# Kernel tuning notes

Measured on AMD Instinct MI355X. Metric: run time of the kernel, lower is better.

Reference implementation:

```python
import jax, jax.numpy as jnp
import numpy as np
import math

B, L, D, P = 2, 2048, 256, 32
PI = math.pi


def _layernorm(x, g, b, eps=1e-5):
    m = x.mean(-1, keepdims=True)
    v = x.var(-1, keepdims=True)
    return (x - m) / jnp.sqrt(v + eps) * g + b


def setup_inputs() -> dict:
    key = jax.random.key(0)
    ks = jax.random.split(key, 16)
    sd = 1.0 / math.sqrt(D)
    f32 = jnp.float32
    inp = {
        "x": jax.random.normal(ks[0], (B, L, D), f32),
        # key_encoder: Linear(D, P)
        "key_W": jax.random.normal(ks[1], (D, P), f32) * sd,
        "key_b": jnp.zeros((P,), f32),
        # value_encoder: Linear(D, D)
        "val_W": jax.random.normal(ks[2], (D, D), f32) * sd,
        "val_b": jnp.zeros((D,), f32),
        # refiner: LayerNorm(D), Linear(D, 2D), GELU, Linear(2D, D)
        "ln1_g": jnp.ones((D,), f32),
        "ln1_b": jnp.zeros((D,), f32),
        "W1": jax.random.normal(ks[3], (D, 2 * D), f32) * sd,
        "b1": jnp.zeros((2 * D,), f32),
        "W2": jax.random.normal(ks[4], (2 * D, D), f32) * (1.0 / math.sqrt(2 * D)),
        "b2": jnp.zeros((D,), f32),
        # to_out: LayerNorm(D), Linear(D, D)
        "ln2_g": jnp.ones((D,), f32),
        "ln2_b": jnp.zeros((D,), f32),
        "Wo": jax.random.normal(ks[5], (D, D), f32) * sd,
        "bo": jnp.zeros((D,), f32),
    }
    return inp


def reference(x, key_W, key_b, val_W, val_b, ln1_g, ln1_b, W1, b1, W2, b2,
              ln2_g, ln2_b, Wo, bo):
    # key phases in (-pi, pi); phasor exp(i*theta) handled as (cos, sin)
    phases = jnp.tanh(x @ key_W + key_b) * PI          # (B, L, P)
    values = x @ val_W + val_b                          # (B, L, D)

    cos_p = jnp.cos(phases)
    sin_p = jnp.sin(phases)
    # torch.roll(shifts=1, dims=1) then zero the first position -> shift right, row 0 = 0
    zrow = jnp.zeros_like(cos_p[:, :1])
    cos_s = jnp.concatenate([zrow, cos_p[:, :-1]], axis=1)
    sin_s = jnp.concatenate([zrow, sin_p[:, :-1]], axis=1)

    # odd positions hold values
    vmask = (jnp.arange(L) % 2 == 1).astype(x.dtype)    # (L,)
    mv = values * vmask[None, :, None]                  # (B, L, D)

    # bind: outer product phasor (P) x value (D); real/imag parts
    bound_re = cos_s[..., None] * mv[:, :, None, :]     # (B, L, P, D)
    bound_im = sin_s[..., None] * mv[:, :, None, :]
    mem_re = jnp.cumsum(bound_re, axis=1)
    mem_im = jnp.cumsum(bound_im, axis=1)

    # retrieve: Re[ memory * exp(-i*theta) ] summed over phases
    retrieved = (jnp.einsum('blpd,blp->bld', mem_re, cos_p)
                 + jnp.einsum('blpd,blp->bld', mem_im, sin_p))

    valid = jnp.maximum(jnp.cumsum(vmask), 1.0)         # (L,)
    retrieved = retrieved / (jnp.sqrt(valid)[None, :, None] * math.sqrt(P))

    h = _layernorm(retrieved, ln1_g, ln1_b)
    h = jax.nn.gelu(h @ W1 + b1, approximate=False)
    refined = h @ W2 + b2
    out = x + (_layernorm(refined, ln2_g, ln2_b) @ Wo + bo)
    return out
```

## Files before the change

kernel.cpp:

```cpp
#include <hip/hip_runtime.h>
#include <math.h>

#define BB 2
#define LL 2048
#define DD 256
#define PP 32
#define NC 64
#define PI_F 3.14159265358979323846f

typedef __attribute__((ext_vector_type(8))) short bf16x8;
typedef __attribute__((ext_vector_type(4))) float f32x4;
typedef unsigned short ushort_t;
typedef unsigned int uint_t;

__device__ inline ushort_t f2bf(float x) {
    uint_t u = __float_as_uint(x);
    uint_t r = (u + 0x7fffu + ((u >> 16) & 1u)) >> 16;
    return (ushort_t)r;
}

__global__ __launch_bounds__(256) void prep_key_kernel(
    const float* __restrict__ W1, const float* __restrict__ W2,
    const float* __restrict__ Wo, const float* __restrict__ valW,
    const float* __restrict__ x, const float* __restrict__ key_W,
    const float* __restrict__ key_b,
    ushort_t* __restrict__ W1t, ushort_t* __restrict__ W2t,
    ushort_t* __restrict__ Wot, ushort_t* __restrict__ valWt,
    float2* __restrict__ ph)
{
    const int bid = blockIdx.x;
    const int t = threadIdx.x;
    if (bid < 96) {
        __shared__ float T[64][65];
        const float* W; ushort_t* Wt; int K, N, tile;
        if (bid < 32)      { W = W1;   Wt = W1t;   K = 256; N = 512; tile = bid; }
        else if (bid < 64) { W = W2;   Wt = W2t;   K = 512; N = 256; tile = bid - 32; }
        else if (bid < 80) { W = Wo;   Wt = Wot;   K = 256; N = 256; tile = bid - 64; }
        else               { W = valW; Wt = valWt; K = 256; N = 256; tile = bid - 80; }
        const int ntiles = N / 64;
        const int k0 = (tile / ntiles) * 64, n0 = (tile % ntiles) * 64;
        {
            const int rr = t >> 2, cb = (t & 3) * 16;
            #pragma unroll
            for (int i = 0; i < 16; i += 4) {
                const float4 v = *(const float4*)&W[(k0 + rr) * N + n0 + cb + i];
                T[rr][cb + i + 0] = v.x; T[rr][cb + i + 1] = v.y;
                T[rr][cb + i + 2] = v.z; T[rr][cb + i + 3] = v.w;
            }
        }
        __syncthreads();
        {
            const int n = t >> 2, kb = (t & 3) * 16;
            #pragma unroll
            for (int i = 0; i < 16; ++i)
                Wt[(n0 + n) * K + k0 + kb + i] = f2bf(T[kb + i][n]);
        }
    } else {
        __shared__ ushort_t xt[16][264];
        __shared__ ushort_t kwT[32][264];
        __shared__ float rbuf[4][2][16][17];
        const int row0 = (bid - 96) * 16;
        {
            const int l = t >> 4, cb = (t & 15) * 16;
            const float* src = &x[(long)(row0 + l) * DD + cb];
            ushort_t tmp[16];
            #pragma unroll
            for (int i = 0; i < 4; ++i) {
                const float4 v = *(const float4*)&src[i * 4];
                tmp[i*4+0] = f2bf(v.x); tmp[i*4+1] = f2bf(v.y);
                tmp[i*4+2] = f2bf(v.z); tmp[i*4+3] = f2bf(v.w);
            }
            *(uint4*)&xt[l][cb]     = *(uint4*)&tmp[0];
            *(uint4*)&xt[l][cb + 8] = *(uint4*)&tmp[8];
        }
        {
            #pragma unroll
            for (int i = 0; i < 8; ++i) {
                const int idx4 = i * 256 + t;
                const int k = idx4 >> 3, pc = (idx4 & 7) * 4;
                const float4 v = *(const float4*)&key_W[k * 32 + pc];
                kwT[pc + 0][k] = f2bf(v.x);
                kwT[pc + 1][k] = f2bf(v.y);
                kwT[pc + 2][k] = f2bf(v.z);
                kwT[pc + 3][k] = f2bf(v.w);
            }
        }
        __syncthreads();
        const int wv = t >> 6, lane = t & 63;
        const int qd = lane >> 4, mc = lane & 15;
        f32x4 acc0 = {0.f,0.f,0.f,0.f}, acc1 = {0.f,0.f,0.f,0.f};
        #pragma unroll
        for (int ks = 0; ks < 2; ++ks) {
            const int ko = wv * 64 + ks * 32 + qd * 8;
            const bf16x8 a  = *(const bf16x8*)&xt[mc][ko];
            const bf16x8 b0 = *(const bf16x8*)&kwT[mc][ko];
            const bf16x8 b1 = *(const bf16x8*)&kwT[16 + mc][ko];
            acc0 = __builtin_amdgcn_mfma_f32_16x16x32_bf16(a, b0, acc0, 0, 0, 0);
            acc1 = __builtin_amdgcn_mfma_f32_16x16x32_bf16(a, b1, acc1, 0, 0, 0);
        }
        #pragma unroll
        for (int r = 0; r < 4; ++r) {
            rbuf[wv][0][qd * 4 + r][mc] = acc0[r];
            rbuf[wv][1][qd * 4 + r][mc] = acc1[r];
        }
        __syncthreads();
        #pragma unroll
        for (int rep = 0; rep < 2; ++rep) {
            const int idx = rep * 256 + t;
            const int p = idx & 31, l = idx >> 5;
            const int nf = p >> 4, mcol = p & 15;
            float a = key_b[p] + rbuf[0][nf][l][mcol] + rbuf[1][nf][l][mcol]
                    + rbuf[2][nf][l][mcol] + rbuf[3][nf][l][mcol];
            a = tanhf(a) * PI_F;
            float sn, cs;
            sincosf(a, &sn, &cs);
            ph[(long)(row0 + l) * PP + p] = make_float2(cs, sn);
        }
    }
}

__global__ __launch_bounds__(256) void valbind_kernel(
    const float* __restrict__ x, const float2* __restrict__ ph,
    const ushort_t* __restrict__ valWt, const float* __restrict__ val_b,
    ushort_t* __restrict__ VoddT, float* __restrict__ Mt)
{
    __shared__ ushort_t xsb[16][264];
    __shared__ ushort_t VdT[64][40];
    __shared__ ushort_t phsT[64][40];
    __shared__ float    Ms[64][68];

    const int tid = threadIdx.x;
    const int bid = blockIdx.x;
    const int b  = bid >> 8;
    const int c  = (bid >> 2) & 63;
    const int dq = bid & 3;
    const int base = b * LL;
    const int r0 = 32 * c;

    {
        const int j = tid >> 4, cb = (tid & 15) * 16;
        const float* src = &x[(long)(base + r0 + 2 * j + 1) * DD + cb];
        ushort_t tmp[16];
        #pragma unroll
        for (int i = 0; i < 4; ++i) {
            const float4 v = *(const float4*)&src[i * 4];
            tmp[i*4+0] = f2bf(v.x); tmp[i*4+1] = f2bf(v.y);
            tmp[i*4+2] = f2bf(v.z); tmp[i*4+3] = f2bf(v.w);
        }
        *(uint4*)&xsb[j][cb]     = *(uint4*)&tmp[0];
        *(uint4*)&xsb[j][cb + 8] = *(uint4*)&tmp[8];
    }
    {
        const int j = tid >> 4, qb = (tid & 15) * 4;
        const float4 v = *(const float4*)((const float*)ph +
                              (long)(base + r0 + 2 * j) * 64 + qb);
        phsT[qb + 0][j] = f2bf(v.x);
        phsT[qb + 1][j] = f2bf(v.y);
        phsT[qb + 2][j] = f2bf(v.z);
        phsT[qb + 3][j] = f2bf(v.w);
    }
    for (int e = tid; e < 64 * 16; e += 256) {
        phsT[e >> 4][16 + (e & 15)] = 0;
        VdT[e >> 4][16 + (e & 15)] = 0;
    }
    __syncthreads();

    const int wv = tid >> 6, lane = tid & 63;
    const int qd = lane >> 4, mc = lane & 15;

    f32x4 va = {0.f,0.f,0.f,0.f};
    const int dloc = wv * 16 + mc;
    const int ng = dq * 64 + dloc;
    const ushort_t* B0 = &valWt[(long)ng * 256];
    #pragma unroll
    for (int ks = 0; ks < 8; ++ks) {
        const bf16x8 a  = *(const bf16x8*)&xsb[mc][ks * 32 + qd * 8];
        const bf16x8 b0 = *(const bf16x8*)&B0[ks * 32 + qd * 8];
        va = __builtin_amdgcn_mfma_f32_16x16x32_bf16(a, b0, va, 0, 0, 0);
    }
    {
        const float bb = val_b[ng];
        #pragma unroll
        for (int r = 0; r < 4; ++r)
            VdT[dloc][qd * 4 + r] = f2bf(va[r] + bb);
    }
    __syncthreads();

    const bf16x8 a2 = *(const bf16x8*)&phsT[wv * 16 + mc][qd * 8];
    f32x4 macc[4];
    #pragma unroll
    for (int nf = 0; nf < 4; ++nf) {
        f32x4 z = {0.f,0.f,0.f,0.f};
        const bf16x8 b2 = *(const bf16x8*)&VdT[nf * 16 + mc][qd * 8];
        macc[nf] = __builtin_amdgcn_mfma_f32_16x16x32_bf16(a2, b2, z, 0, 0, 0);
    }
    #pragma unroll
    for (int nf = 0; nf < 4; ++nf) {
        #pragma unroll
        for (int r = 0; r < 4; ++r)
            Ms[nf * 16 + mc][wv * 16 + qd * 4 + r] = macc[nf][r];
    }
    __syncthreads();

    {
        float* dst = &Mt[((long)(b * NC + c) * 256 + dq * 64) * 64];
        #pragma unroll
        for (int p = 0; p < 4; ++p) {
            const int idx4 = p * 256 + tid;
            const int dl = idx4 >> 4, q4 = (idx4 & 15) * 4;
            *(float4*)&dst[dl * 64 + q4] = *(const float4*)&Ms[dl][q4];
        }
    }
    if (tid < 64) {
        ushort_t* vd = &VoddT[((long)(b * NC + c) * 256 + dq * 64 + tid) * 16];
        *(uint4*)&vd[0] = *(const uint4*)&VdT[tid][0];
        *(uint4*)&vd[8] = *(const uint4*)&VdT[tid][8];
    }
}

__global__ __launch_bounds__(256) void prefix_kernel(
    const float* __restrict__ M, ushort_t* __restrict__ Mpre_b)
{
    __shared__ float segsum[4][64];
    const int tid = threadIdx.x;
    const int b  = blockIdx.x >> 8;
    const int cg = blockIdx.x & 255;
    const int col = cg * 64 + (tid & 63);
    const int seg = tid >> 6;
    const long base = (long)b * NC * 16384 + col;

    float v[16], s = 0.f;
    #pragma unroll
    for (int i = 0; i < 16; ++i) {
        v[i] = M[base + (long)(seg * 16 + i) * 16384];
        s += v[i];
    }
    segsum[seg][tid & 63] = s;
    __syncthreads();
    float run = 0.f;
    #pragma unroll
    for (int sg = 0; sg < 3; ++sg)
        if (sg < seg) run += segsum[sg][tid & 63];
    #pragma unroll
    for (int i = 0; i < 16; ++i) {
        const long a = base + (long)(seg * 16 + i) * 16384;
        Mpre_b[a] = f2bf(run);
        run += v[i];
    }
}

__global__ __launch_bounds__(512) void retrieve_mlp_kernel(
    const float* __restrict__ ph, const ushort_t* __restrict__ Mpre_b,
    const ushort_t* __restrict__ VoddT,
    const float* __restrict__ ln1_g, const float* __restrict__ ln1_b,
    const ushort_t* __restrict__ W1t, const float* __restrict__ b1,
    const ushort_t* __restrict__ W2t, const float* __restrict__ b2,
    const float* __restrict__ ln2_g, const float* __restrict__ ln2_b,
    const ushort_t* __restrict__ Wot, const float* __restrict__ bo,
    const float* __restrict__ x, float* __restrict__ out)
{
    __shared__ ushort_t Bs_m[256][72];
    __shared__ ushort_t Bs_v[256][32];
    __shared__ ushort_t As_ph[16][72];
    __shared__ ushort_t Bs_sh[16][72];
    __shared__ ushort_t As_p[16][32];
    __shared__ float    refct[16][264];
    __shared__ ushort_t rhat_s[16][264];
    __shared__ ushort_t h_s[16][520];
    __shared__ ushort_t shT[16][264];

    const int tid = threadIdx.x;
    const int b = blockIdx.x >> 7;
    const int c = (blockIdx.x >> 1) & 63;
    const int h = blockIdx.x & 1;
    const int l0g = 32 * c + 16 * h;
    const long rowbase = (long)b * LL + l0g;

    {
        const ushort_t* src = &Mpre_b[(long)(b * NC + c) * 16384];
        #pragma unroll
        for (int p = 0; p < 4; ++p) {
            const int idx8 = p * 512 + tid;
            const int d = idx8 >> 3, q8 = (idx8 & 7) * 8;
            *(uint4*)&Bs_m[d][q8] = *(const uint4*)&src[idx8 * 8];
        }
    }
    if (tid < 256) {
        const int r = tid >> 4, q4 = (tid & 15) * 4;
        const float4 vv = *(const float4*)((const float*)ph + (rowbase + r) * 64 + q4);
        ushort_t t0[4] = {f2bf(vv.x), f2bf(vv.y), f2bf(vv.z), f2bf(vv.w)};
        *(uint2*)&As_ph[r][q4] = *(uint2*)t0;
        const float4 w = *(const float4*)((const float*)ph +
                             ((long)b * LL + 32 * c + 2 * r) * 64 + q4);
        ushort_t t1[4] = {f2bf(w.x), f2bf(w.y), f2bf(w.z), f2bf(w.w)};
        *(uint2*)&Bs_sh[r][q4] = *(uint2*)t1;
    }
    {
        const ushort_t* src = &VoddT[(long)(b * NC + c) * 4096];
        const int j0 = (tid & 1) * 8;
        *(uint4*)&Bs_v[tid >> 1][j0] = *(const uint4*)&src[tid * 8];
        *(uint4*)&Bs_v[tid >> 1][16 + j0] = make_uint4(0, 0, 0, 0);
        if (tid < 256) As_p[tid >> 4][16 + (tid & 15)] = 0;
    }
    __syncthreads();

    const int wv = tid >> 6, lane = tid & 63;
    const int qd = lane >> 4, mc = lane & 15;

    {
        f32x4 sacc = {0.f, 0.f, 0.f, 0.f};
        #pragma unroll
        for (int ks = 0; ks < 2; ++ks) {
            const bf16x8 a  = *(const bf16x8*)&As_ph[mc][ks * 32 + qd * 8];
            const bf16x8 bb = *(const bf16x8*)&Bs_sh[mc][ks * 32 + qd * 8];
            sacc = __builtin_amdgcn_mfma_f32_16x16x32_bf16(a, bb, sacc, 0, 0, 0);
        }
        if (wv == 0) {
            #pragma unroll
            for (int r = 0; r < 4; ++r) {
                const int l = qd * 4 + r;
                As_p[l][mc] = (2 * mc + 1 <= 16 * h + l) ? f2bf(sacc[r])
                                                         : (ushort_t)0;
            }
        }
    }

    f32x4 acc[2];
    #pragma unroll
    for (int i = 0; i < 2; ++i) acc[i] = (f32x4){0.f, 0.f, 0.f, 0.f};
    #pragma unroll
    for (int i = 0; i < 2; ++i) {
        const int d0 = wv * 32 + i * 16;
        #pragma unroll
        for (int ks = 0; ks < 2; ++ks) {
            const bf16x8 a  = *(const bf16x8*)&As_ph[mc][ks * 32 + qd * 8];
            const bf16x8 bb = *(const bf16x8*)&Bs_m[d0 + mc][ks * 32 + qd * 8];
            acc[i] = __builtin_amdgcn_mfma_f32_16x16x32_bf16(a, bb, acc[i], 0, 0, 0);
        }
    }
    __syncthreads();

    {
        const bf16x8 a2 = *(const bf16x8*)&As_p[mc][qd * 8];
        #pragma unroll
        for (int i = 0; i < 2; ++i) {
            const int d0 = wv * 32 + i * 16;
            const bf16x8 b2 = *(const bf16x8*)&Bs_v[d0 + mc][qd * 8];
            acc[i] = __builtin_amdgcn_mfma_f32_16x16x32_bf16(a2, b2, acc[i], 0, 0, 0);
        }
    }

    #pragma unroll
    for (int r = 0; r < 4; ++r) {
        const int l = qd * 4 + r;
        int va = (l0g + l + 1) >> 1; if (va < 1) va = 1;
        const float sc = 0.17677669529663687f * rsqrtf((float)va);
        #pragma unroll
        for (int i = 0; i < 2; ++i)
            refct[l][wv * 32 + i * 16 + mc] = acc[i][r] * sc;
    }
    __syncthreads();

    {
        const int row = tid >> 5, cg = (tid & 31) * 8;
        float s = 0.f, sq = 0.f;
        #pragma unroll
        for (int i = 0; i < 8; ++i) {
            const float v = refct[row][cg + i];
            s += v; sq += v * v;
        }
        s += __shfl_xor(s, 1, 32);  sq += __shfl_xor(sq, 1, 32);
        s += __shfl_xor(s, 2, 32);  sq += __shfl_xor(sq, 2, 32);
        s += __shfl_xor(s, 4, 32);  sq += __shfl_xor(sq, 4, 32);
        s += __shfl_xor(s, 8, 32);  sq += __shfl_xor(sq, 8, 32);
        s += __shfl_xor(s, 16, 32); sq += __shfl_xor(sq, 16, 32);
        const float m = s * (1.f / 256.f);
        const float inv = rsqrtf(sq * (1.f / 256.f) - m * m + 1e-5f);
        ushort_t o16[8];
        #pragma unroll
        for (int i = 0; i < 8; ++i) {
            const int cc = cg + i;
            o16[i] = f2bf((refct[row][cc] - m) * inv * ln1_g[cc] + ln1_b[cc]);
        }
        *(uint4*)&rhat_s[row][cg] = *(uint4*)&o16[0];
    }

    #pragma unroll
    for (int nh = 0; nh < 2; ++nh) {
        f32x4 acc1[2];
        #pragma unroll
        for (int nf = 0; nf < 2; ++nf) acc1[nf] = (f32x4){0.f,0.f,0.f,0.f};
        for (int k0 = 0; k0 < 256; k0 += 64) {
            __syncthreads();
            {
                const int sk = (tid & 7) * 8;
                #pragma unroll
                for (int rr = 0; rr < 4; ++rr) {
                    const int n = rr * 64 + (tid >> 3);
                    *(uint4*)&Bs_m[n][sk] =
                        *(const uint4*)&W1t[(long)(nh * 256 + n) * 256 + k0 + sk];
                }
            }
            __syncthreads();
            #pragma unroll
            for (int ks = 0; ks < 2; ++ks) {
                const bf16x8 a = *(const bf16x8*)&rhat_s[mc][k0 + ks * 32 + qd * 8];
                #pragma unroll
                for (int nf = 0; nf < 2; ++nf) {
                    const bf16x8 bb = *(const bf16x8*)&Bs_m[wv * 32 + nf * 16 + mc][ks * 32 + qd * 8];
                    acc1[nf] = __builtin_amdgcn_mfma_f32_16x16x32_bf16(a, bb, acc1[nf], 0, 0, 0);
                }
            }
        }
        #pragma unroll
        for (int nf = 0; nf < 2; ++nf) {
            const int n = nh * 256 + wv * 32 + nf * 16 + mc;
            const float bb = b1[n];
            #pragma unroll
            for (int r = 0; r < 4; ++r) {
                float v = acc1[nf][r] + bb;
                v = 0.5f * v * (1.f + erff(v * 0.70710678118654752f));
                h_s[qd * 4 + r][n] = f2bf(v);
            }
        }
    }

    f32x4 acc2[2];
    #pragma unroll
    for (int nf = 0; nf < 2; ++nf) acc2[nf] = (f32x4){0.f,0.f,0.f,0.f};
    for (int k0 = 0; k0 < 512; k0 += 64) {
        __syncthreads();
        {
            const int sk = (tid & 7) * 8;
            #pragma unroll
            for (int rr = 0; rr < 4; ++rr) {
                const int n = rr * 64 + (tid >> 3);
                *(uint4*)&Bs_m[n][sk] = *(const uint4*)&W2t[(long)n * 512 + k0 + sk];
            }
        }
        __syncthreads();
        #pragma unroll
        for (int ks = 0; ks < 2; ++ks) {
            const bf16x8 a = *(const bf16x8*)&h_s[mc][k0 + ks * 32 + qd * 8];
            #pragma unroll
            for (int nf = 0; nf < 2; ++nf) {
                const bf16x8 bb = *(const bf16x8*)&Bs_m[wv * 32 + nf * 16 + mc][ks * 32 + qd * 8];
                acc2[nf] = __builtin_amdgcn_mfma_f32_16x16x32_bf16(a, bb, acc2[nf], 0, 0, 0);
            }
        }
    }
    #pragma unroll
    for (int nf = 0; nf < 2; ++nf) {
        const int n = wv * 32 + nf * 16 + mc;
        const float bb = b2[n];
        #pragma unroll
        for (int r = 0; r < 4; ++r)
            refct[qd * 4 + r][n] = acc2[nf][r] + bb;
    }
    __syncthreads();

    {
        const int row = tid >> 5, cg = (tid & 31) * 8;
        float s = 0.f, sq = 0.f;
        #pragma unroll
        for (int i = 0; i < 8; ++i) {
            const float v = refct[row][cg + i];
            s += v; sq += v * v;
        }
        s += __shfl_xor(s, 1, 32);  sq += __shfl_xor(sq, 1, 32);
        s += __shfl_xor(s, 2, 32);  sq += __shfl_xor(sq, 2, 32);
        s += __shfl_xor(s, 4, 32);  sq += __shfl_xor(sq, 4, 32);
        s += __shfl_xor(s, 8, 32);  sq += __shfl_xor(sq, 8, 32);
        s += __shfl_xor(s, 16, 32); sq += __shfl_xor(sq, 16, 32);
        const float m = s * (1.f / 256.f);
        const float inv = rsqrtf(sq * (1.f / 256.f) - m * m + 1e-5f);
        ushort_t o16[8];
        #pragma unroll
        for (int i = 0; i < 8; ++i) {
            const int cc = cg + i;
            o16[i] = f2bf((refct[row][cc] - m) * inv * ln2_g[cc] + ln2_b[cc]);
        }
        *(uint4*)&shT[row][cg] = *(uint4*)&o16[0];
    }

    f32x4 acc3[2];
    #pragma unroll
    for (int nf = 0; nf < 2; ++nf) acc3[nf] = (f32x4){0.f,0.f,0.f,0.f};
    for (int k0 = 0; k0 < 256; k0 += 64) {
        __syncthreads();
        {
            const int sk = (tid & 7) * 8;
            #pragma unroll
            for (int rr = 0; rr < 4; ++rr) {
                const int n = rr * 64 + (tid >> 3);
                *(uint4*)&Bs_m[n][sk] = *(const uint4*)&Wot[(long)n * 256 + k0 + sk];
            }
        }
        __syncthreads();
        #pragma unroll
        for (int ks = 0; ks < 2; ++ks) {
            const bf16x8 a = *(const bf16x8*)&shT[mc][k0 + ks * 32 + qd * 8];
            #pragma unroll
            for (int nf = 0; nf < 2; ++nf) {
                const bf16x8 bb = *(const bf16x8*)&Bs_m[wv * 32 + nf * 16 + mc][ks * 32 + qd * 8];
                acc3[nf] = __builtin_amdgcn_mfma_f32_16x16x32_bf16(a, bb, acc3[nf], 0, 0, 0);
            }
        }
    }
    #pragma unroll
    for (int nf = 0; nf < 2; ++nf) {
        const int n = wv * 32 + nf * 16 + mc;
        const float bb = bo[n];
        #pragma unroll
        for (int r = 0; r < 4; ++r) {
            const long row = rowbase + qd * 4 + r;
            out[row * DD + n] = acc3[nf][r] + bb + x[row * DD + n];
        }
    }
}

extern "C" void kernel_launch(void* const* d_in, const int* in_sizes, int n_in,
                              void* d_out, int out_size, void* d_ws, size_t ws_size,
                              hipStream_t stream)
{
    const float* x     = (const float*)d_in[0];
    const float* key_W = (const float*)d_in[1];
    const float* key_b = (const float*)d_in[2];
    const float* val_W = (const float*)d_in[3];
    const float* val_b = (const float*)d_in[4];
    const float* ln1_g = (const float*)d_in[5];
    const float* ln1_b = (const float*)d_in[6];
    const float* W1    = (const float*)d_in[7];
    const float* b1    = (const float*)d_in[8];
    const float* W2    = (const float*)d_in[9];
    const float* b2    = (const float*)d_in[10];
    const float* ln2_g = (const float*)d_in[11];
    const float* ln2_b = (const float*)d_in[12];
    const float* Wo    = (const float*)d_in[13];
    const float* bo    = (const float*)d_in[14];
    float* outp = (float*)d_out;

    float* ws = (float*)d_ws;
    float*  ph      = ws;
    float*  Mt      = ws + 262144;
    ushort_t* Mpre_b = (ushort_t*)(Mt + 2097152);
    ushort_t* VoddT  = Mpre_b + 2097152;
    ushort_t* rhat_b = VoddT + 524288;
    ushort_t* W1t   = rhat_b + 1048576;
    ushort_t* W2t   = W1t + 131072;
    ushort_t* Wot   = W2t + 131072;
    ushort_t* valWt = Wot + 65536;

    prep_key_kernel<<<352, 256, 0, stream>>>(W1, W2, Wo, val_W, x, key_W, key_b,
                                             W1t, W2t, Wot, valWt, (float2*)ph);
    valbind_kernel<<<512, 256, 0, stream>>>(x, (const float2*)ph, valWt, val_b,
                                            VoddT, Mt);
    prefix_kernel<<<512, 256, 0, stream>>>(Mt, Mpre_b);
    retrieve_mlp_kernel<<<256, 512, 0, stream>>>(ph, Mpre_b, VoddT, ln1_g, ln1_b,
                                                 W1t, b1, W2t, b2, ln2_g, ln2_b,
                                                 Wot, bo, x, outp);
}
```

Measured before the change: 123.7 us.

## Register-prefetch next weight tile across the three MLP GEMM stages

Weight tiles for the W1, W2 and Wo GEMMs are now loaded one iteration ahead into registers and stored to shared memory at the start of the next iteration. The prefetch chain also crosses stage boundaries: the first W2 tile is fetched during the last W1 step, and the first Wo tile during the last W2 step. This hides global-load latency behind the MFMA work and the LayerNorm/GELU epilogues, which were previously serialized by the syncthreads around each load. The cost is extra registers per thread, which could reduce occupancy.

```diff
diff --git a/kernel.cpp b/kernel.cpp
--- a/kernel.cpp
+++ b/kernel.cpp
@@ -306,6 +306,7 @@
 
     const int wv = tid >> 6, lane = tid & 63;
     const int qd = lane >> 4, mc = lane & 15;
+    const int sk = (tid & 7) * 8, nrow = tid >> 3;
 
     {
         f32x4 sacc = {0.f, 0.f, 0.f, 0.f};
@@ -360,6 +361,11 @@
             refct[l][wv * 32 + i * 16 + mc] = acc[i][r] * sc;
     }
     __syncthreads();
+
+    uint4 pre[4];
+    #pragma unroll
+    for (int rr = 0; rr < 4; ++rr)
+        pre[rr] = *(const uint4*)&W1t[(long)(rr * 64 + nrow) * 256 + sk];
 
     {
         const int row = tid >> 5, cg = (tid & 31) * 8;
@@ -385,21 +391,26 @@
         *(uint4*)&rhat_s[row][cg] = *(uint4*)&o16[0];
     }
 
-    #pragma unroll
-    for (int nh = 0; nh < 2; ++nh) {
+    {
         f32x4 acc1[2];
-        #pragma unroll
-        for (int nf = 0; nf < 2; ++nf) acc1[nf] = (f32x4){0.f,0.f,0.f,0.f};
-        for (int k0 = 0; k0 < 256; k0 += 64) {
+        acc1[0] = (f32x4){0.f,0.f,0.f,0.f};
+        acc1[1] = (f32x4){0.f,0.f,0.f,0.f};
+        #pragma unroll
+        for (int it = 0; it < 8; ++it) {
+            const int k0 = (it & 3) * 64;
             __syncthreads();
-            {
-                const int sk = (tid & 7) * 8;
+            #pragma unroll
+            for (int rr = 0; rr < 4; ++rr)
+                *(uint4*)&Bs_m[rr * 64 + nrow][sk] = pre[rr];
+            if (it < 7) {
+                const int nhn = (it + 1) >> 2, k0n = ((it + 1) & 3) * 64;
                 #pragma unroll
-                for (int rr = 0; rr < 4; ++rr) {
-                    const int n = rr * 64 + (tid >> 3);
-                    *(uint4*)&Bs_m[n][sk] =
-                        *(const uint4*)&W1t[(long)(nh * 256 + n) * 256 + k0 + sk];
-                }
+                for (int rr = 0; rr < 4; ++rr)
+                    pre[rr] = *(const uint4*)&W1t[(long)(nhn * 256 + rr * 64 + nrow) * 256 + k0n + sk];
+            } else {
+                #pragma unroll
+                for (int rr = 0; rr < 4; ++rr)
+                    pre[rr] = *(const uint4*)&W2t[(long)(rr * 64 + nrow) * 512 + sk];
             }
             __syncthreads();
             #pragma unroll
@@ -411,32 +422,42 @@
                     acc1[nf] = __builtin_amdgcn_mfma_f32_16x16x32_bf16(a, bb, acc1[nf], 0, 0, 0);
                 }
             }
-        }
-        #pragma unroll
-        for (int nf = 0; nf < 2; ++nf) {
-            const int n = nh * 256 + wv * 32 + nf * 16 + mc;
-            const float bb = b1[n];
-            #pragma unroll
-            for (int r = 0; r < 4; ++r) {
-                float v = acc1[nf][r] + bb;
-                v = 0.5f * v * (1.f + erff(v * 0.70710678118654752f));
-                h_s[qd * 4 + r][n] = f2bf(v);
+            if ((it & 3) == 3) {
+                const int nh = it >> 2;
+                #pragma unroll
+                for (int nf = 0; nf < 2; ++nf) {
+                    const int n = nh * 256 + wv * 32 + nf * 16 + mc;
+                    const float bb = b1[n];
+                    #pragma unroll
+                    for (int r = 0; r < 4; ++r) {
+                        float v = acc1[nf][r] + bb;
+                        v = 0.5f * v * (1.f + erff(v * 0.70710678118654752f));
+                        h_s[qd * 4 + r][n] = f2bf(v);
+                    }
+                    acc1[nf] = (f32x4){0.f,0.f,0.f,0.f};
+                }
             }
         }
     }
 
     f32x4 acc2[2];
-    #pragma unroll
-    for (int nf = 0; nf < 2; ++nf) acc2[nf] = (f32x4){0.f,0.f,0.f,0.f};
-    for (int k0 = 0; k0 < 512; k0 += 64) {
-        __syncthreads();
-        {
-            const int sk = (tid & 7) * 8;
-            #pragma unroll
-            for (int rr = 0; rr < 4; ++rr) {
-                const int n = rr * 64 + (tid >> 3);
-                *(uint4*)&Bs_m[n][sk] = *(const uint4*)&W2t[(long)n * 512 + k0 + sk];
-            }
+    acc2[0] = (f32x4){0.f,0.f,0.f,0.f};
+    acc2[1] = (f32x4){0.f,0.f,0.f,0.f};
+    #pragma unroll
+    for (int it = 0; it < 8; ++it) {
+        const int k0 = it * 64;
+        __syncthreads();
+        #pragma unroll
+        for (int rr = 0; rr < 4; ++rr)
+            *(uint4*)&Bs_m[rr * 64 + nrow][sk] = pre[rr];
+        if (it < 7) {
+            #pragma unroll
+            for (int rr = 0; rr < 4; ++rr)
+                pre[rr] = *(const uint4*)&W2t[(long)(rr * 64 + nrow) * 512 + k0 + 64 + sk];
+        } else {
+            #pragma unroll
+            for (int rr = 0; rr < 4; ++rr)
+                pre[rr] = *(const uint4*)&Wot[(long)(rr * 64 + nrow) * 256 + sk];
         }
         __syncthreads();
         #pragma unroll
@@ -484,17 +505,19 @@
     }
 
     f32x4 acc3[2];
-    #pragma unroll
-    for (int nf = 0; nf < 2; ++nf) acc3[nf] = (f32x4){0.f,0.f,0.f,0.f};
-    for (int k0 = 0; k0 < 256; k0 += 64) {
-        __syncthreads();
-        {
-            const int sk = (tid & 7) * 8;
-            #pragma unroll
-            for (int rr = 0; rr < 4; ++rr) {
-                const int n = rr * 64 + (tid >> 3);
-                *(uint4*)&Bs_m[n][sk] = *(const uint4*)&Wot[(long)n * 256 + k0 + sk];
-            }
+    acc3[0] = (f32x4){0.f,0.f,0.f,0.f};
+    acc3[1] = (f32x4){0.f,0.f,0.f,0.f};
+    #pragma unroll
+    for (int it = 0; it < 4; ++it) {
+        const int k0 = it * 64;
+        __syncthreads();
+        #pragma unroll
+        for (int rr = 0; rr < 4; ++rr)
+            *(uint4*)&Bs_m[rr * 64 + nrow][sk] = pre[rr];
+        if (it < 3) {
+            #pragma unroll
+            for (int rr = 0; rr < 4; ++rr)
+                pre[rr] = *(const uint4*)&Wot[(long)(rr * 64 + nrow) * 256 + k0 + 64 + sk];
         }
         __syncthreads();
         #pragma unroll
```

Result: slower. 153.1 us (+23.8%).
